# Optimization experiments

Measured on AMD Instinct MI355X. Metric: run time of the kernel, lower is better.

Reference implementation:

```python
import jax, jax.numpy as jnp
import numpy as np

B, N, M = 4, 1024, 100
NB = 25
NTYPE = 2
TYPES = (1, 8)
FEAT = NB * NTYPE  # 50
H = 100
PI = 3.1415926
RMIN, RMAX = 0.5, 6.0


def setup_inputs() -> dict:
    key = jax.random.key(0)
    ks = jax.random.split(key, 12)
    type_map = jnp.array(TYPES)
    Imagetype = type_map[jax.random.randint(ks[0], (B, N), 0, NTYPE)]
    neighbor_list = jax.random.randint(ks[1], (B, N, M), 0, N + 1)
    rij = jax.random.uniform(ks[2], (B, N, M), minval=0.5, maxval=7.0)
    d = jax.random.normal(ks[3], (B, N, M, 3))
    d = d / jnp.linalg.norm(d, axis=-1, keepdims=True)
    ImagedR = jnp.concatenate([rij[..., None], d * rij[..., None]], axis=-1).astype(jnp.float32)

    def w(k, i, o):
        return (jax.random.normal(k, (NTYPE, i, o)) / np.sqrt(i + o)).astype(jnp.float32)

    def b(k, o):
        return jax.random.normal(k, (NTYPE, o)).astype(jnp.float32)

    return {"Imagetype": Imagetype, "neighbor_list": neighbor_list, "ImagedR": ImagedR,
            "W0": w(ks[4], FEAT, H), "b0": b(ks[5], H),
            "W1": w(ks[6], H, H), "b1": b(ks[7], H),
            "W2": w(ks[8], H, H), "b2": b(ks[9], H),
            "W3": w(ks[10], H, 1), "b3": b(ks[11], 1)}


def _net(x, W0, b0, W1, b1, W2, b2, W3, b3):
    # NET with network_size [50,100,100,100,1], tanh, resnet_dt=False
    h = jnp.tanh(x @ W0 + b0)
    x = h + jnp.concatenate([x, x], axis=-1)  # 50 -> 100 doubling skip
    h = jnp.tanh(x @ W1 + b1); x = h + x
    h = jnp.tanh(x @ W2 + b2); x = h + x
    return x @ W3 + b3


def _body2fun(Imagetype, neighbor_list, ImagedR):
    Bn, Nn, Mn = neighbor_list.shape
    rs = jnp.linspace(RMIN, RMAX, NB)  # [NB]
    r = ImagedR[..., 0]  # [B,N,M]
    rb = jnp.broadcast_to(r[..., None], (Bn, Nn, Mn, NB))

    def fc_fn(rt):
        env = jnp.exp(-(rt - rs) ** 2) * (0.5 * jnp.cos(PI * rt) + 0.5)
        return jnp.where((rt < RMAX) & (rt > 0), env, 0.0)

    # dfc = d(fc)/dr, elementwise, matching torch.autograd.grad with ones
    fc, dfc = jax.jvp(fc_fn, (rb,), (jnp.ones_like(rb),))

    # neighbor_type: 1-indexed lookup with 0 -> padding type 0
    padded = jnp.concatenate([jnp.zeros((Bn, 1), Imagetype.dtype), Imagetype], axis=1)
    nt = jnp.take_along_axis(padded, neighbor_list.reshape(Bn, -1), axis=1).reshape(Bn, Nn, Mn)

    dvec = jnp.where(r[..., None] != 0, ImagedR[..., 1:4] / r[..., None], 0.0)  # [B,N,M,3]

    feats, dfeats = [], []
    for t in TYPES:
        m = (nt == t)[..., None]  # [B,N,M,1]
        fct = jnp.where(m, fc, 0.0)
        dfct = jnp.where(m, dfc, 0.0)
        feats.append(fct.sum(axis=2))  # [B,N,NB]
        dfeats.append(dfct[..., None] * dvec[..., None, :])  # [B,N,M,NB,3]
    feat = jnp.concatenate(feats, axis=-1)  # [B,N,50]
    dfeat = jnp.concatenate(dfeats, axis=3)  # [B,N,M,50,3]
    return feat, dfeat


def reference(Imagetype, neighbor_list, ImagedR, W0, b0, W1, b1, W2, b2, W3, b3):
    Bn, Nn, Mn = neighbor_list.shape
    feat, dfeat = _body2fun(Imagetype, neighbor_list, ImagedR)

    type_arr = jnp.array(TYPES)
    mask = (Imagetype[None] == type_arr[:, None, None])[..., None]  # [T,B,N,1]

    def ei_fn(f):
        e = jax.vmap(_net, in_axes=(None, 0, 0, 0, 0, 0, 0, 0, 0))(
            f, W0, b0, W1, b1, W2, b2, W3, b3)  # [T,B,N,1]
        return jnp.sum(jnp.where(mask, e, 0.0), axis=0)  # [B,N,1]

    Ei = ei_fn(feat)
    Etot = jnp.sum(Ei, axis=1)  # [B,1]

    # dE/dfeat of total energy (grad_outputs = ones on Etot)
    dE = jax.grad(lambda f: jnp.sum(ei_fn(f)))(feat)  # [B,N,50]

    dE_Rid = jnp.einsum('bnf,bnmfc->bnmc', dE, dfeat)  # [B,N,M,3]
    Force = -dE_Rid.sum(axis=2)  # [B,N,3]

    # scatter-add of neighbor contributions: segment 0 is padding
    seg = jax.vmap(lambda v, i: jax.ops.segment_sum(v, i, num_segments=Nn + 1))(
        dE_Rid.reshape(Bn, -1, 3), neighbor_list.reshape(Bn, -1))  # [B,N+1,3]
    Force = Force + seg[:, 1:, :]
    return Etot, Ei, Force
```

## Files before the change

### kernel.cpp

```cpp
#include <hip/hip_runtime.h>

#define Bn   4
#define Nn   1024
#define Mn   100
#define NB   25
#define FEAT 50
#define PIc  3.1415926f
#define RSTEP (5.5f / 24.0f)

#define ATB  16
#define NATOMS (Bn * Nn)
#define ORDER_LEN (NATOMS + ATB)
#define MLP_BLOCKS (ORDER_LEN / ATB)
#define TYW  122880

#define GPB  64
#define CPG  16
#define FTHREADS 512

typedef __attribute__((ext_vector_type(8))) short bf16x8;
typedef __attribute__((ext_vector_type(4))) float f32x4;

union U16x8 { unsigned short u[8]; bf16x8 v; uint4 q; };

__device__ __forceinline__ unsigned short f2bh(float x) {
    union { float f; unsigned u; } v; v.f = x;
    unsigned r = v.u + 0x7fffu + ((v.u >> 16) & 1u);
    return (unsigned short)(r >> 16);
}
__device__ __forceinline__ float bh2f(unsigned short h) {
    union { unsigned u; float f; } v; v.u = ((unsigned)h) << 16; return v.f;
}
__device__ __forceinline__ float fast_tanh(float x) {
    float ax = fabsf(x);
    float t  = __expf(-2.0f * ax);
    float r  = (1.0f - t) * __builtin_amdgcn_rcpf(1.0f + t);
    return copysignf(r, x);
}


__global__ __launch_bounds__(256) void wprep_kernel(
    const int* __restrict__ itype,
    const float* __restrict__ W0, const float* __restrict__ W1,
    const float* __restrict__ W2,
    int* __restrict__ order, unsigned short* __restrict__ wsu)
{
    const int blk = blockIdx.x;
    const int t = threadIdx.x;

    if (blk < 20) {
        __shared__ float tile[64][65];
        int ty = blk / 10, m = blk - ty * 10;
        int mat, jt, kt;
        if (m < 2)      { mat = 0; jt = m;            kt = 0; }
        else if (m < 6) { mat = 1; jt = (m - 2) >> 1; kt = (m - 2) & 1; }
        else            { mat = 2; jt = (m - 6) >> 1; kt = (m - 6) & 1; }
        const float* src = (mat == 0) ? W0 + ty * 5000
                          : (mat == 1) ? W1 + ty * 10000 : W2 + ty * 10000;
        const int Krows = (mat == 0) ? 50 : 100;
        const int Ck    = (mat == 0) ? 64 : 128;
        const int dH = ty * TYW + ((mat == 0) ? 0 : (mat == 1) ? 16384 : 49152);
        const int dL = dH + ((mat == 0) ? 8192 : 16384);
        const int j0 = jt * 64, k0 = kt * 64;
        const int rr0 = t >> 6, l = t & 63;
        #pragma unroll
        for (int i = 0; i < 16; ++i) {
            int rr = rr0 + 4 * i;
            int k = k0 + rr, j = j0 + l;
            tile[rr][l] = (k < Krows && j < 100) ? src[k * 100 + j] : 0.0f;
        }
        __syncthreads();
        #pragma unroll
        for (int i = 0; i < 16; ++i) {
            int jj = rr0 + 4 * i;
            float v = tile[l][jj];
            unsigned short h = f2bh(v);
            wsu[dH + (j0 + jj) * Ck + k0 + l] = h;
            wsu[dL + (j0 + jj) * Ck + k0 + l] = f2bh(v - bh2f(h));
        }
        return;
    }
    if (blk < 340) {
        int e = (blk - 20) * 256 + t;
        int ty = e / 40960;
        int r  = e - ty * 40960;
        float v = 0.0f; int dst;
        if (r < 16384) {
            int i = r >> 7, j = r & 127;
            if (i < 100 && j < 100) v = W2[ty * 10000 + i * 100 + j];
            dst = ty * TYW + 81920 + r;
        } else if (r < 32768) {
            int r2 = r - 16384; int i = r2 >> 7, j = r2 & 127;
            if (i < 100 && j < 100) v = W1[ty * 10000 + i * 100 + j];
            dst = ty * TYW + 98304 + r2;
        } else {
            int r2 = r - 32768; int f = r2 >> 7, j = r2 & 127;
            if (f < 50 && j < 100) v = W0[ty * 5000 + f * 100 + j];
            dst = ty * TYW + 114688 + r2;
        }
        wsu[dst] = f2bh(v);
        return;
    }
    __shared__ int scan[256];
    for (int i = t; i < ORDER_LEN; i += 256) order[i] = -1;
    int tyv[16]; int c0 = 0;
    #pragma unroll
    for (int k = 0; k < 16; ++k) {
        int tt = (itype[t * 16 + k] == 8) ? 1 : 0;
        tyv[k] = tt; c0 += 1 - tt;
    }
    scan[t] = c0;
    __syncthreads();
    for (int off = 1; off < 256; off <<= 1) {
        int v = scan[t];
        int add = (t >= off) ? scan[t - off] : 0;
        __syncthreads();
        scan[t] = v + add;
        __syncthreads();
    }
    int total0 = scan[255];
    int ex0 = scan[t] - c0;
    int ex1 = 16 * t - ex0;
    int pad0 = (total0 + (ATB - 1)) & ~(ATB - 1);
    int p0 = ex0, p1 = pad0 + ex1;
    #pragma unroll
    for (int k = 0; k < 16; ++k) {
        int idx = t * 16 + k;
        if (tyv[k] == 0) order[p0++] = idx; else order[p1++] = idx;
    }
}

__global__ __launch_bounds__(128) void feat_kernel(
    const int* __restrict__ itype, const int* __restrict__ nlist,
    const float* __restrict__ dR, float* __restrict__ featp)
{
    const int atom = blockIdx.x;
    const int b = atom >> 10;
    const int t = threadIdx.x;

    __shared__ float4 rc4[50];
    __shared__ float partial[64];

    if (t < Mn) {
        float4 qv = ((const float4*)dR)[(size_t)atom * Mn + t];
        float r = qv.x;
        int v = nlist[(size_t)atom * Mn + t];
        float cws = 0.0f;
        if (v > 0 && r > 0.0f && r < 6.0f) {
            float cw = 0.5f * __cosf(PIc * r) + 0.5f;
            cws = (itype[b * Nn + (v - 1)] == 8) ? -cw : cw;
        }
        ((float2*)rc4)[t] = make_float2(r, cws);
    }
    __syncthreads();

    const int w = t >> 6, l = t & 63;
    const int tt = l / NB;
    const float rk = 0.5f + (l - tt * NB) * RSTEP;
    float acc = 0.0f;
    #pragma unroll
    for (int i = 0; i < 25; ++i) {
        float4 pr = rc4[w * 25 + i];
        float d0 = pr.x - rk, d1 = pr.z - rk;
        float c0 = tt ? fmaxf(-pr.y, 0.0f) : fmaxf(pr.y, 0.0f);
        float c1 = tt ? fmaxf(-pr.w, 0.0f) : fmaxf(pr.w, 0.0f);
        acc += __expf(-d0 * d0) * c0 + __expf(-d1 * d1) * c1;
    }
    if (w == 1) partial[l] = acc;
    __syncthreads();
    if (w == 0) {
        float tot = (l < FEAT) ? (acc + partial[l]) : 0.0f;
        featp[(size_t)atom * 64 + l] = tot;
    }
}

#define ISSUE(RH, RL, OFFU, OFFL, RW, NKT, HASLO, COND)                       \
    if (COND) {                                                               \
        int jj_ = c + 16 * w;                                                 \
        _Pragma("unroll")                                                     \
        for (int kt = 0; kt < (NKT); ++kt) {                                  \
            int boff_ = jj_ * (RW) + kt * 32 + q * 8;                         \
            RH[kt] = *(const bf16x8*)(wb + (OFFU) + boff_);                   \
            if (HASLO) RL[kt] = *(const bf16x8*)(wb + (OFFL) + boff_);        \
        }                                                                     \
    }

#define GEMM_R(ABUF, RH, RL, NKT, HASLO)                                      \
    {                                                                         \
        acc = (f32x4){0,0,0,0}; accl = (f32x4){0,0,0,0};                      \
        _Pragma("unroll")                                                     \
        for (int kt = 0; kt < (NKT); ++kt) {                                  \
            int gk = kt * 4 + q;                                              \
            bf16x8 af = *(const bf16x8*)&aA[ABUF][(c << 7) | ((gk ^ (c & 7)) << 3)]; \
            acc = __builtin_amdgcn_mfma_f32_16x16x32_bf16(af, RH[kt], acc, 0, 0, 0); \
            if (HASLO) accl = __builtin_amdgcn_mfma_f32_16x16x32_bf16(af, RL[kt], accl, 0, 0, 0); \
        }                                                                     \
    }

#define WRACT(BUF, J, A, X)                                                   \
    aA[BUF][((A) << 7) | ((((J) >> 3) ^ ((A) & 7)) << 3) | ((J) & 7)] = f2bh(X)

__global__ __launch_bounds__(512) void mlp_kernel(
    const float* __restrict__ featp, const int* __restrict__ itype,
    const int* __restrict__ order, const unsigned short* __restrict__ wsu,
    const float* __restrict__ B0, const float* __restrict__ B1,
    const float* __restrict__ B2, const float* __restrict__ W3,
    const float* __restrict__ B3,
    float* __restrict__ Ei, float* __restrict__ dE)
{
    const int t = threadIdx.x;
    const int w = t >> 6;
    const int lane = t & 63;
    const int c = lane & 15, q = lane >> 4;

    __shared__ unsigned short aA[2][2048];
    __shared__ float fshf[16][52];
    __shared__ float dx1s[16][112];
    __shared__ float biasS[4][128];
    __shared__ float eip[8][16];
    __shared__ int aid[16];

    if (t < 16) aid[t] = order[blockIdx.x * ATB + t];
    __syncthreads();
    int first = -1;
    #pragma unroll
    for (int a = 0; a < ATB; ++a) { int v = aid[a]; if (first < 0 && v >= 0) first = v; }
    if (first < 0) return;
    const int ty = (itype[first] == 8) ? 1 : 0;
    const unsigned short* wb = wsu + (size_t)ty * TYW;

    bf16x8 bh0[4], bl0[4], bh1[4], bl1[4];
    f32x4 acc, accl;
    float xr[4], h0r[4], h1r[4], h2r[4], dxr[4];

    ISSUE(bh0, bl0, 0, 8192, 64, 2, 1, true);
    if (t < 128) {
        const int srow = t >> 3, sg = t & 7;
        int v = aid[srow];
        float4 fa = {0,0,0,0}, fb = {0,0,0,0};
        if (v >= 0) {
            const float4* fp = (const float4*)(featp + (size_t)v * 64 + sg * 8);
            fa = fp[0]; fb = fp[1];
        }
        U16x8 pk;
        pk.u[0]=f2bh(fa.x); pk.u[1]=f2bh(fa.y); pk.u[2]=f2bh(fa.z); pk.u[3]=f2bh(fa.w);
        pk.u[4]=f2bh(fb.x); pk.u[5]=f2bh(fb.y); pk.u[6]=f2bh(fb.z); pk.u[7]=f2bh(fb.w);
        *(uint4*)&aA[0][(srow << 7) | ((sg ^ (srow & 7)) << 3)] = pk.q;
        int cbase = sg * 8;
        if (cbase < 52) {
            float vals[8] = {fa.x,fa.y,fa.z,fa.w,fb.x,fb.y,fb.z,fb.w};
            #pragma unroll
            for (int j7 = 0; j7 < 8; ++j7)
                if (cbase + j7 < 52) fshf[srow][cbase + j7] = vals[j7];
        }
    }
    if (t < 512) {
        int row = t >> 7, col = t & 127;
        const float* s = (row == 0) ? B0 : (row == 1) ? B1 : (row == 2) ? B2 : W3;
        biasS[row][col] = (col < 100) ? s[ty * 100 + col] : 0.0f;
    }
    __syncthreads();

    ISSUE(bh1, bl1, 16384, 32768, 128, 4, 1, true);
    GEMM_R(0, bh0, bl0, 2, 1);
    {
        int j = c + 16 * w;
        float bj = biasS[0][j];
        #pragma unroll
        for (int r = 0; r < 4; ++r) {
            int a = q * 4 + r;
            float z = acc[r] + accl[r] + bj;
            float h = 0.f, x = 0.f;
            if (j < 100) { h = fast_tanh(z); x = h + fshf[a][(j < 50) ? j : j - 50]; }
            h0r[r] = h; xr[r] = x;
            WRACT(1, j, a, x);
        }
    }
    __syncthreads();

    ISSUE(bh0, bl0, 49152, 65536, 128, 4, 1, true);
    GEMM_R(1, bh1, bl1, 4, 1);
    {
        int j = c + 16 * w;
        float bj = biasS[1][j];
        #pragma unroll
        for (int r = 0; r < 4; ++r) {
            int a = q * 4 + r;
            float z = acc[r] + accl[r] + bj;
            float h = (j < 100) ? fast_tanh(z) : 0.f;
            float x = (j < 100) ? (h + xr[r]) : 0.f;
            h1r[r] = h; xr[r] = x;
            WRACT(0, j, a, x);
        }
    }
    __syncthreads();

    ISSUE(bh1, bl1, 81920, 0, 128, 4, 0, true);
    GEMM_R(0, bh0, bl0, 4, 1);
    {
        int j = c + 16 * w;
        float bj = biasS[2][j];
        float wv = biasS[3][j];
        float p4v[4];
        #pragma unroll
        for (int r = 0; r < 4; ++r) {
            float z = acc[r] + accl[r] + bj;
            float h = (j < 100) ? fast_tanh(z) : 0.f;
            h2r[r] = h;
            xr[r] = (j < 100) ? (h + xr[r]) : 0.f;
            p4v[r] = xr[r] * wv;
        }
        #pragma unroll
        for (int off = 1; off < 16; off <<= 1) {
            #pragma unroll
            for (int r = 0; r < 4; ++r) p4v[r] += __shfl_xor(p4v[r], off);
        }
        if (c == 0) {
            #pragma unroll
            for (int r = 0; r < 4; ++r) eip[w][q * 4 + r] = p4v[r];
        }
        #pragma unroll
        for (int r = 0; r < 4; ++r) {
            int a = q * 4 + r;
            float d = wv * (1.0f - h2r[r] * h2r[r]);
            WRACT(1, j, a, d);
        }
    }
    __syncthreads();
    if (t < 16) {
        int v = aid[t];
        if (v >= 0) {
            float e = B3[ty];
            #pragma unroll
            for (int ww = 0; ww < 8; ++ww) e += eip[ww][t];
            Ei[v] = e;
        }
    }

    ISSUE(bh0, bl0, 98304, 0, 128, 4, 0, true);
    GEMM_R(1, bh1, bl1, 4, 0);
    {
        int i = c + 16 * w;
        float w3i = biasS[3][i];
        #pragma unroll
        for (int r = 0; r < 4; ++r) {
            int a = q * 4 + r;
            float dx2 = acc[r] + w3i;
            dxr[r] = dx2;
            float d = dx2 * (1.0f - h1r[r] * h1r[r]);
            WRACT(0, i, a, d);
        }
    }
    __syncthreads();

    ISSUE(bh1, bl1, 114688, 0, 128, 4, 0, (w < 4));
    GEMM_R(0, bh0, bl0, 4, 0);
    {
        int i = c + 16 * w;
        #pragma unroll
        for (int r = 0; r < 4; ++r) {
            int a = q * 4 + r;
            float dx1 = dxr[r] + acc[r];
            if (i < 112) dx1s[a][i] = dx1;
            float d = dx1 * (1.0f - h0r[r] * h0r[r]);
            WRACT(1, i, a, d);
        }
    }
    __syncthreads();

    if (w < 4) {
        GEMM_R(1, bh1, bl1, 4, 0);
        int f = c + 16 * w;
        if (f < 50) {
            #pragma unroll
            for (int r = 0; r < 4; ++r) {
                int a = q * 4 + r;
                int v = aid[a];
                if (v >= 0) dE[(size_t)v * FEAT + f] = acc[r] + dx1s[a][f] + dx1s[a][f + 50];
            }
        }
    }
}

__global__ __launch_bounds__(FTHREADS) void force_kernel(
    const int* __restrict__ itype, const int* __restrict__ nlist,
    const float* __restrict__ dR, const float* __restrict__ dE,
    float* __restrict__ partial)
{
    const int blk = blockIdx.x;
    const int b = blk / GPB;
    const int g = blk - b * GPB;
    const int t = threadIdx.x;

    __shared__ float acc[(Nn + 1) * 3];
    __shared__ float desh[CPG][FEAT];

    for (int idx = t; idx < (Nn + 1) * 3; idx += FTHREADS) acc[idx] = 0.0f;
    for (int idx = t; idx < CPG * FEAT; idx += FTHREADS)
        ((float*)desh)[idx] = dE[((size_t)(b * Nn) + g * CPG) * FEAT + idx];
    __syncthreads();

    for (int p = t; p < CPG * Mn; p += FTHREADS) {
        int cc = p / Mn, m = p - cc * Mn;
        int n = g * CPG + cc;
        size_t pair = (size_t)(b * Nn + n) * Mn + m;
        float4 qv = ((const float4*)dR)[pair];
        int v = nlist[pair];
        if (v > 0) {
            float r = qv.x;
            if (r > 0.0f && r < 6.0f) {
                int tt = (itype[b * Nn + v - 1] == 8) ? 1 : 0;
                float cw  = 0.5f * __cosf(PIc * r) + 0.5f;
                float dcw = -0.5f * PIc * __sinf(PIc * r);
                float s = 0.0f;
                const float* de = &desh[cc][tt * NB];
                #pragma unroll
                for (int k = 0; k < NB; ++k) {
                    float d = r - (0.5f + k * RSTEP);
                    float e = __expf(-d * d);
                    s += de[k] * e * __builtin_fmaf(-2.0f * cw, d, dcw);
                }
                float inv = 1.0f / r;
                float fx = s * qv.y * inv, fy = s * qv.z * inv, fz = s * qv.w * inv;
                atomicAdd(&acc[v * 3 + 0], fx);
                atomicAdd(&acc[v * 3 + 1], fy);
                atomicAdd(&acc[v * 3 + 2], fz);
                atomicAdd(&acc[(n + 1) * 3 + 0], -fx);
                atomicAdd(&acc[(n + 1) * 3 + 1], -fy);
                atomicAdd(&acc[(n + 1) * 3 + 2], -fz);
            }
        }
    }
    __syncthreads();

    float* pout = partial + (size_t)blk * ((Nn + 1) * 3);
    for (int idx = t; idx < (Nn + 1) * 3; idx += FTHREADS) pout[idx] = acc[idx];
}

__global__ __launch_bounds__(256) void freduce_kernel(
    const float* __restrict__ partial, const float* __restrict__ Ei,
    float* __restrict__ Force, float* __restrict__ Etot)
{
    if (blockIdx.x == 48) {
        const int t = threadIdx.x;
        __shared__ float red[256];
        for (int b = 0; b < Bn; ++b) {
            float s = 0.0f;
            for (int i = t; i < Nn; i += 256) s += Ei[b * Nn + i];
            red[t] = s;
            __syncthreads();
            for (int st = 128; st > 0; st >>= 1) {
                if (t < st) red[t] += red[t + st];
                __syncthreads();
            }
            if (t == 0) Etot[b] = red[0];
            __syncthreads();
        }
        return;
    }
    int idx = blockIdx.x * 256 + threadIdx.x;
    if (idx >= Bn * Nn * 3) return;
    int b = idx / (Nn * 3);
    int r = idx - b * (Nn * 3);
    int i = r / 3, ch = r - i * 3;
    float s = 0.0f;
    for (int g = 0; g < GPB; ++g)
        s += partial[((size_t)(b * GPB + g)) * ((Nn + 1) * 3) + (size_t)(i + 1) * 3 + ch];
    Force[idx] = s;
}

extern "C" void kernel_launch(void* const* d_in, const int* in_sizes, int n_in,
                              void* d_out, int out_size, void* d_ws, size_t ws_size,
                              hipStream_t stream)
{
    const int*   itype = (const int*)d_in[0];
    const int*   nlist = (const int*)d_in[1];
    const float* dR    = (const float*)d_in[2];
    const float* W0 = (const float*)d_in[3];  const float* B0 = (const float*)d_in[4];
    const float* W1 = (const float*)d_in[5];  const float* B1 = (const float*)d_in[6];
    const float* W2 = (const float*)d_in[7];  const float* B2 = (const float*)d_in[8];
    const float* W3 = (const float*)d_in[9];  const float* B3 = (const float*)d_in[10];

    float* out   = (float*)d_out;
    float* Etot  = out;
    float* Ei    = out + Bn;
    float* Force = out + Bn + Bn * Nn;

    float* featp   = (float*)d_ws;
    float* dEp     = featp + (size_t)NATOMS * 64;
    float* partial = dEp + (size_t)NATOMS * FEAT;
    int*   order   = (int*)(partial + (size_t)Bn * GPB * (Nn + 1) * 3);
    unsigned short* wsu = (unsigned short*)(order + ORDER_LEN);

    wprep_kernel  <<<341, 256, 0, stream>>>(itype, W0, W1, W2, order, wsu);
    feat_kernel   <<<NATOMS, 128, 0, stream>>>(itype, nlist, dR, featp);
    mlp_kernel    <<<MLP_BLOCKS, 512, 0, stream>>>(featp, itype, order, wsu,
                                                   B0, B1, B2, W3, B3, Ei, dEp);
    force_kernel  <<<Bn * GPB, FTHREADS, 0, stream>>>(itype, nlist, dR, dEp, partial);
    freduce_kernel<<<49, 256, 0, stream>>>(partial, Ei, Force, Etot);
}
```

Baseline: 59.65 us.

## Fuse feature computation into MLP and replace partial-force reduction with atomics

Removes the separate feature kernel: each MLP block now loads its atoms' neighbor pairs into shared memory and computes the 50 radial features in place, avoiding the featp round trip through global memory and one launch. The force kernel now uses 8 groups per batch instead of 64 and atomically adds its shared-memory accumulator straight into Force. That removes the partial buffer and the separate reduce kernel; Force is zeroed in the prep kernel, and the Etot sum moves into an extra force block. The cost is less parallelism in the force stage and feature work serialized inside the MLP blocks, plus global atomic contention.

```diff
diff --git a/kernel.cpp b/kernel.cpp
--- a/kernel.cpp
+++ b/kernel.cpp
@@ -14,8 +14,8 @@
 #define MLP_BLOCKS (ORDER_LEN / ATB)
 #define TYW  122880
 
-#define GPB  64
-#define CPG  16
+#define GPB  8
+#define CPG  128
 #define FTHREADS 512
 
 typedef __attribute__((ext_vector_type(8))) short bf16x8;
@@ -39,11 +39,12 @@
 }
 
 
-__global__ __launch_bounds__(256) void wprep_kernel(
+__global__ __launch_bounds__(256) void prep_kernel(
     const int* __restrict__ itype,
     const float* __restrict__ W0, const float* __restrict__ W1,
     const float* __restrict__ W2,
-    int* __restrict__ order, unsigned short* __restrict__ wsu)
+    int* __restrict__ order, unsigned short* __restrict__ wsu,
+    float* __restrict__ Force)
 {
     const int blk = blockIdx.x;
     const int t = threadIdx.x;
@@ -101,6 +102,11 @@
         wsu[dst] = f2bh(v);
         return;
     }
+    if (blk < 388) {
+        int idx = (blk - 340) * 256 + t;
+        if (idx < Bn * Nn * 3) Force[idx] = 0.0f;
+        return;
+    }
     __shared__ int scan[256];
     for (int i = t; i < ORDER_LEN; i += 256) order[i] = -1;
     int tyv[16]; int c0 = 0;
@@ -127,50 +133,6 @@
     for (int k = 0; k < 16; ++k) {
         int idx = t * 16 + k;
         if (tyv[k] == 0) order[p0++] = idx; else order[p1++] = idx;
-    }
-}
-
-__global__ __launch_bounds__(128) void feat_kernel(
-    const int* __restrict__ itype, const int* __restrict__ nlist,
-    const float* __restrict__ dR, float* __restrict__ featp)
-{
-    const int atom = blockIdx.x;
-    const int b = atom >> 10;
-    const int t = threadIdx.x;
-
-    __shared__ float4 rc4[50];
-    __shared__ float partial[64];
-
-    if (t < Mn) {
-        float4 qv = ((const float4*)dR)[(size_t)atom * Mn + t];
-        float r = qv.x;
-        int v = nlist[(size_t)atom * Mn + t];
-        float cws = 0.0f;
-        if (v > 0 && r > 0.0f && r < 6.0f) {
-            float cw = 0.5f * __cosf(PIc * r) + 0.5f;
-            cws = (itype[b * Nn + (v - 1)] == 8) ? -cw : cw;
-        }
-        ((float2*)rc4)[t] = make_float2(r, cws);
-    }
-    __syncthreads();
-
-    const int w = t >> 6, l = t & 63;
-    const int tt = l / NB;
-    const float rk = 0.5f + (l - tt * NB) * RSTEP;
-    float acc = 0.0f;
-    #pragma unroll
-    for (int i = 0; i < 25; ++i) {
-        float4 pr = rc4[w * 25 + i];
-        float d0 = pr.x - rk, d1 = pr.z - rk;
-        float c0 = tt ? fmaxf(-pr.y, 0.0f) : fmaxf(pr.y, 0.0f);
-        float c1 = tt ? fmaxf(-pr.w, 0.0f) : fmaxf(pr.w, 0.0f);
-        acc += __expf(-d0 * d0) * c0 + __expf(-d1 * d1) * c1;
-    }
-    if (w == 1) partial[l] = acc;
-    __syncthreads();
-    if (w == 0) {
-        float tot = (l < FEAT) ? (acc + partial[l]) : 0.0f;
-        featp[(size_t)atom * 64 + l] = tot;
     }
 }
 
@@ -201,7 +163,8 @@
     aA[BUF][((A) << 7) | ((((J) >> 3) ^ ((A) & 7)) << 3) | ((J) & 7)] = f2bh(X)
 
 __global__ __launch_bounds__(512) void mlp_kernel(
-    const float* __restrict__ featp, const int* __restrict__ itype,
+    const float* __restrict__ dR, const int* __restrict__ nlist,
+    const int* __restrict__ itype,
     const int* __restrict__ order, const unsigned short* __restrict__ wsu,
     const float* __restrict__ B0, const float* __restrict__ B1,
     const float* __restrict__ B2, const float* __restrict__ W3,
@@ -213,6 +176,7 @@
     const int lane = t & 63;
     const int c = lane & 15, q = lane >> 4;
 
+    __shared__ float2 pairsh[ATB * Mn];
     __shared__ unsigned short aA[2][2048];
     __shared__ float fshf[16][52];
     __shared__ float dx1s[16][112];
@@ -234,30 +198,55 @@
     float xr[4], h0r[4], h1r[4], h2r[4], dxr[4];
 
     ISSUE(bh0, bl0, 0, 8192, 64, 2, 1, true);
-    if (t < 128) {
-        const int srow = t >> 3, sg = t & 7;
-        int v = aid[srow];
-        float4 fa = {0,0,0,0}, fb = {0,0,0,0};
+
+    for (int p = t; p < ATB * Mn; p += 512) {
+        int a = p / Mn, m = p - a * Mn;
+        int v = aid[a];
+        float2 pr = make_float2(0.0f, 0.0f);
         if (v >= 0) {
-            const float4* fp = (const float4*)(featp + (size_t)v * 64 + sg * 8);
-            fa = fp[0]; fb = fp[1];
-        }
-        U16x8 pk;
-        pk.u[0]=f2bh(fa.x); pk.u[1]=f2bh(fa.y); pk.u[2]=f2bh(fa.z); pk.u[3]=f2bh(fa.w);
-        pk.u[4]=f2bh(fb.x); pk.u[5]=f2bh(fb.y); pk.u[6]=f2bh(fb.z); pk.u[7]=f2bh(fb.w);
-        *(uint4*)&aA[0][(srow << 7) | ((sg ^ (srow & 7)) << 3)] = pk.q;
-        int cbase = sg * 8;
-        if (cbase < 52) {
-            float vals[8] = {fa.x,fa.y,fa.z,fa.w,fb.x,fb.y,fb.z,fb.w};
-            #pragma unroll
-            for (int j7 = 0; j7 < 8; ++j7)
-                if (cbase + j7 < 52) fshf[srow][cbase + j7] = vals[j7];
-        }
-    }
-    if (t < 512) {
+            float4 qv = ((const float4*)dR)[(size_t)v * Mn + m];
+            int nb = nlist[(size_t)v * Mn + m];
+            float r = qv.x;
+            if (nb > 0 && r > 0.0f && r < 6.0f) {
+                float cw = 0.5f * __cosf(PIc * r) + 0.5f;
+                pr = make_float2(r, (itype[(v >> 10) * Nn + nb - 1] == 8) ? -cw : cw);
+            } else pr.x = r;
+        }
+        pairsh[p] = pr;
+    }
+    {
         int row = t >> 7, col = t & 127;
         const float* s = (row == 0) ? B0 : (row == 1) ? B1 : (row == 2) ? B2 : W3;
         biasS[row][col] = (col < 100) ? s[ty * 100 + col] : 0.0f;
+    }
+    __syncthreads();
+
+    for (int u = t; u < ATB * FEAT; u += 512) {
+        int a = u / FEAT, l = u - a * FEAT;
+        int tt = l / NB;
+        float rk = 0.5f + (l - tt * NB) * RSTEP;
+        float s = 0.0f;
+        const float2* pp = &pairsh[a * Mn];
+        #pragma unroll 4
+        for (int m = 0; m < Mn; ++m) {
+            float2 pr = pp[m];
+            float cc = tt ? fmaxf(-pr.y, 0.0f) : fmaxf(pr.y, 0.0f);
+            float d = pr.x - rk;
+            s += __expf(-d * d) * cc;
+        }
+        fshf[a][l] = s;
+    }
+    __syncthreads();
+
+    if (t < 128) {
+        const int srow = t >> 3, sg = t & 7;
+        U16x8 pk;
+        #pragma unroll
+        for (int j7 = 0; j7 < 8; ++j7) {
+            int k = sg * 8 + j7;
+            pk.u[j7] = (k < FEAT) ? f2bh(fshf[srow][k]) : 0;
+        }
+        *(uint4*)&aA[0][(srow << 7) | ((sg ^ (srow & 7)) << 3)] = pk.q;
     }
     __syncthreads();
 
@@ -385,12 +374,31 @@
 __global__ __launch_bounds__(FTHREADS) void force_kernel(
     const int* __restrict__ itype, const int* __restrict__ nlist,
     const float* __restrict__ dR, const float* __restrict__ dE,
-    float* __restrict__ partial)
+    const float* __restrict__ Ei,
+    float* __restrict__ Force, float* __restrict__ Etot)
 {
     const int blk = blockIdx.x;
+    const int t = threadIdx.x;
+
+    if (blk == Bn * GPB) {
+        __shared__ float red[FTHREADS];
+        for (int b = 0; b < Bn; ++b) {
+            float s = 0.0f;
+            for (int i = t; i < Nn; i += FTHREADS) s += Ei[b * Nn + i];
+            red[t] = s;
+            __syncthreads();
+            for (int st = FTHREADS / 2; st > 0; st >>= 1) {
+                if (t < st) red[t] += red[t + st];
+                __syncthreads();
+            }
+            if (t == 0) Etot[b] = red[0];
+            __syncthreads();
+        }
+        return;
+    }
+
     const int b = blk / GPB;
     const int g = blk - b * GPB;
-    const int t = threadIdx.x;
 
     __shared__ float acc[(Nn + 1) * 3];
     __shared__ float desh[CPG][FEAT];
@@ -433,40 +441,8 @@
     }
     __syncthreads();
 
-    float* pout = partial + (size_t)blk * ((Nn + 1) * 3);
-    for (int idx = t; idx < (Nn + 1) * 3; idx += FTHREADS) pout[idx] = acc[idx];
-}
-
-__global__ __launch_bounds__(256) void freduce_kernel(
-    const float* __restrict__ partial, const float* __restrict__ Ei,
-    float* __restrict__ Force, float* __restrict__ Etot)
-{
-    if (blockIdx.x == 48) {
-        const int t = threadIdx.x;
-        __shared__ float red[256];
-        for (int b = 0; b < Bn; ++b) {
-            float s = 0.0f;
-            for (int i = t; i < Nn; i += 256) s += Ei[b * Nn + i];
-            red[t] = s;
-            __syncthreads();
-            for (int st = 128; st > 0; st >>= 1) {
-                if (t < st) red[t] += red[t + st];
-                __syncthreads();
-            }
-            if (t == 0) Etot[b] = red[0];
-            __syncthreads();
-        }
-        return;
-    }
-    int idx = blockIdx.x * 256 + threadIdx.x;
-    if (idx >= Bn * Nn * 3) return;
-    int b = idx / (Nn * 3);
-    int r = idx - b * (Nn * 3);
-    int i = r / 3, ch = r - i * 3;
-    float s = 0.0f;
-    for (int g = 0; g < GPB; ++g)
-        s += partial[((size_t)(b * GPB + g)) * ((Nn + 1) * 3) + (size_t)(i + 1) * 3 + ch];
-    Force[idx] = s;
+    for (int idx = t; idx < Nn * 3; idx += FTHREADS)
+        atomicAdd(&Force[(size_t)b * Nn * 3 + idx], acc[idx + 3]);
 }
 
 extern "C" void kernel_launch(void* const* d_in, const int* in_sizes, int n_in,
@@ -486,16 +462,13 @@
     float* Ei    = out + Bn;
     float* Force = out + Bn + Bn * Nn;
 
-    float* featp   = (float*)d_ws;
-    float* dEp     = featp + (size_t)NATOMS * 64;
-    float* partial = dEp + (size_t)NATOMS * FEAT;
-    int*   order   = (int*)(partial + (size_t)Bn * GPB * (Nn + 1) * 3);
+    float* dEp   = (float*)d_ws;
+    int*   order = (int*)(dEp + (size_t)NATOMS * FEAT);
     unsigned short* wsu = (unsigned short*)(order + ORDER_LEN);
 
-    wprep_kernel  <<<341, 256, 0, stream>>>(itype, W0, W1, W2, order, wsu);
-    feat_kernel   <<<NATOMS, 128, 0, stream>>>(itype, nlist, dR, featp);
-    mlp_kernel    <<<MLP_BLOCKS, 512, 0, stream>>>(featp, itype, order, wsu,
-                                                   B0, B1, B2, W3, B3, Ei, dEp);
-    force_kernel  <<<Bn * GPB, FTHREADS, 0, stream>>>(itype, nlist, dR, dEp, partial);
-    freduce_kernel<<<49, 256, 0, stream>>>(partial, Ei, Force, Etot);
-}
+    prep_kernel <<<389, 256, 0, stream>>>(itype, W0, W1, W2, order, wsu, Force);
+    mlp_kernel  <<<MLP_BLOCKS, 512, 0, stream>>>(dR, nlist, itype, order, wsu,
+                                                 B0, B1, B2, W3, B3, Ei, dEp);
+    force_kernel<<<Bn * GPB + 1, FTHREADS, 0, stream>>>(itype, nlist, dR, dEp,
+                                                        Ei, Force, Etot);
+}
```

Measured after the change: 144.1 us. 2.42x slower.
